# Optimization experiments

Measured on AMD Instinct MI355X. Metric: run time of the kernel, lower is better.

## Reference

```python
import jax, jax.numpy as jnp
import numpy as np

NUM_GRAPHS = 64

def setup_inputs() -> dict:
    key = jax.random.key(0)
    ks = jax.random.split(key, 10)
    N, E, D, V = 100000, 1600000, 64, 30
    node_types = jax.random.randint(ks[0], (N,), 0, V, dtype=jnp.int64 if jax.config.jax_enable_x64 else jnp.int32)
    edge_index = jax.random.randint(ks[1], (2, E), 0, N, dtype=jnp.int32)
    batch = jnp.sort(jax.random.randint(ks[2], (N,), 0, NUM_GRAPHS, dtype=jnp.int32))
    emb_table = jax.random.normal(ks[3], (V, D), dtype=jnp.float32)
    W1 = jax.random.normal(ks[4], (D, D), dtype=jnp.float32) / np.sqrt(D)
    W2 = jax.random.normal(ks[5], (D, D), dtype=jnp.float32) / np.sqrt(D)
    W3 = jax.random.normal(ks[6], (D, D), dtype=jnp.float32) / np.sqrt(D)
    b1 = jnp.zeros((D,), jnp.float32)
    b2 = jnp.zeros((D,), jnp.float32)
    b3 = jnp.zeros((D,), jnp.float32)
    return {"node_types": node_types, "edge_index": edge_index, "batch": batch,
            "emb_table": emb_table, "W1": W1, "b1": b1, "W2": W2, "b2": b2, "W3": W3, "b3": b3}

def _gcn_conv(x, W, b, row, col, norm, N):
    # x' = D^-1/2 (A+I) D^-1/2 (x @ W) + b   (PyG GCNConv semantics)
    h = x @ W
    msg = h[row] * norm[:, None]              # gather + edgewise scale
    out = jax.ops.segment_sum(msg, col, num_segments=N)  # scatter-add at targets
    return out + b

def reference(node_types, edge_index, batch, emb_table, W1, b1, W2, b2, W3, b3):
    N = node_types.shape[0]
    # add self-loops
    loops = jnp.arange(N, dtype=edge_index.dtype)
    row = jnp.concatenate([edge_index[0], loops])
    col = jnp.concatenate([edge_index[1], loops])
    # symmetric normalization on A + I
    deg = jax.ops.segment_sum(jnp.ones_like(col, dtype=jnp.float32), col, num_segments=N)
    dinv = jnp.where(deg > 0, jax.lax.rsqrt(deg), 0.0)
    norm = dinv[row] * dinv[col]
    x = emb_table[node_types]
    x = jax.nn.relu(_gcn_conv(x, W1, b1, row, col, norm, N))
    x = jax.nn.relu(_gcn_conv(x, W2, b2, row, col, norm, N))
    x = _gcn_conv(x, W3, b3, row, col, norm, N)
    # global mean pool over batch segments
    sums = jax.ops.segment_sum(x, batch, num_segments=NUM_GRAPHS)
    cnts = jax.ops.segment_sum(jnp.ones((N,), jnp.float32), batch, num_segments=NUM_GRAPHS)
    pooled = sums / jnp.maximum(cnts, 1.0)[:, None]
    # L2 normalize rows
    return pooled / jnp.linalg.norm(pooled, axis=1, keepdims=True)
```

## Files before the change

### kernel.cpp

```cpp
#include <hip/hip_runtime.h>
#include <hip/hip_fp16.h>

#define DD 64
#define NUM_GRAPHS 64
#define AGG_BLOCKS 2048
#define EB 512
#define BINW 256
#define MAXNB 512
#define EBIN_CAP 6144

typedef _Float16 h2_t __attribute__((ext_vector_type(2)));

__device__ __forceinline__ float fdot2u(unsigned a, unsigned b, float c) {
    return __builtin_amdgcn_fdot2(__builtin_bit_cast(h2_t, a),
                                  __builtin_bit_cast(h2_t, b), c, false);
}

#define MDLO(m) __half2float(__ushort_as_half((unsigned short)((m) & 0xFFFF)))

__global__ __launch_bounds__(256) void k_hist(const int* __restrict__ col,
                                              int* __restrict__ H, int E, int NB, int CE) {
    __shared__ int h[MAXNB];
    int eb = blockIdx.x, t = threadIdx.x;
    for (int i = t; i < NB; i += 256) h[i] = 0;
    __syncthreads();
    int e0 = eb * CE, e1 = min(E, e0 + CE);
    for (int e = e0 + t; e < e1; e += 256) atomicAdd(&h[col[e] >> 8], 1);
    __syncthreads();
    for (int i = t; i < NB; i += 256) H[eb * NB + i] = h[i];
}

__global__ __launch_bounds__(256) void k_scanA(int* __restrict__ H,
                                               int* __restrict__ bintot, int NB) {
    __shared__ int s[256];
    int b = blockIdx.x, t = threadIdx.x;
    int i0 = (2 * t) * NB + b, i1 = (2 * t + 1) * NB + b;
    int v0 = H[i0], v1 = H[i1];
    int tot = v0 + v1;
    s[t] = tot;
    __syncthreads();
    for (int off = 1; off < 256; off <<= 1) {
        int tv = (t >= off) ? s[t - off] : 0;
        __syncthreads();
        s[t] += tv;
        __syncthreads();
    }
    int excl = s[t] - tot;
    H[i0] = excl;
    H[i1] = excl + v0;
    if (t == 255) bintot[b] = s[255];
}

__global__ void k_scanB(const int* __restrict__ bintot, int* __restrict__ binstart, int NB) {
    __shared__ int s[512];
    int t = threadIdx.x;
    int v = (t < NB) ? bintot[t] : 0;
    s[t] = v;
    __syncthreads();
    for (int off = 1; off < 512; off <<= 1) {
        int tv = (t >= off) ? s[t - off] : 0;
        __syncthreads();
        s[t] += tv;
        __syncthreads();
    }
    if (t < NB) binstart[t] = s[t] - v;
    if (t == 511) binstart[NB] = s[511];
}

__global__ __launch_bounds__(256) void k_scatbin(const int* __restrict__ row,
                                                 const int* __restrict__ col,
                                                 const int* __restrict__ H,
                                                 const int* __restrict__ binstart,
                                                 unsigned* __restrict__ binned,
                                                 int E, int NB, int CE) {
    __shared__ int off[MAXNB];
    int eb = blockIdx.x, t = threadIdx.x;
    for (int i = t; i < NB; i += 256) off[i] = binstart[i] + H[eb * NB + i];
    __syncthreads();
    int e0 = eb * CE, e1 = min(E, e0 + CE);
    for (int e = e0 + t; e < e1; e += 256) {
        int c = col[e], r = row[e];
        int slot = atomicAdd(&off[c >> 8], 1);
        binned[slot] = ((unsigned)(c & 255) << 24) | (unsigned)r;
    }
}

__global__ __launch_bounds__(256) void k_bincsr(const unsigned* __restrict__ binned,
                                                const int* __restrict__ binstart,
                                                const int* __restrict__ nt,
                                                int* __restrict__ srcidx,
                                                int* __restrict__ rowptr,
                                                float* __restrict__ dinv,
                                                int2* __restrict__ pk, int N, int NB) {
    __shared__ unsigned arr[EBIN_CAP];
    __shared__ int sorted_[EBIN_CAP];
    __shared__ int cnt[BINW];
    __shared__ int base[BINW];
    __shared__ int cursor[BINW];
    int b = blockIdx.x, t = threadIdx.x;
    int s0 = binstart[b], s1 = binstart[b + 1];
    int binsz = s1 - s0;
    if (binsz > EBIN_CAP) binsz = EBIN_CAP;
    cnt[t] = 0;
    for (int i = t; i < binsz; i += 256) arr[i] = binned[s0 + i];
    __syncthreads();
    for (int i = t; i < binsz; i += 256) atomicAdd(&cnt[arr[i] >> 24], 1);
    __syncthreads();
    int v = cnt[t];
    base[t] = v;
    __syncthreads();
    for (int off = 1; off < 256; off <<= 1) {
        int tv = (t >= off) ? base[t - off] : 0;
        __syncthreads();
        base[t] += tv;
        __syncthreads();
    }
    int excl = base[t] - v;
    __syncthreads();
    base[t] = excl;
    cursor[t] = excl;
    __syncthreads();
    for (int i = t; i < binsz; i += 256) {
        unsigned val = arr[i];
        int pos = atomicAdd(&cursor[val >> 24], 1);
        sorted_[pos] = (int)(val & 0xFFFFFF);
    }
    __syncthreads();
    for (int i = t; i < binsz; i += 256) srcidx[s0 + i] = sorted_[i];
    int node = b * BINW + t;
    if (node < N) {
        rowptr[node] = s0 + base[t];
        float di = rsqrtf((float)cnt[t] + 1.0f);
        dinv[node] = di;
        pk[node] = make_int2(nt[node], __float_as_int(di));
    }
    if (b == NB - 1 && t == 0) rowptr[N] = s1;
}

__global__ void k_buildepk(const int* __restrict__ srcidx, const int2* __restrict__ pk,
                           unsigned* __restrict__ epku, int E) {
    int i = blockIdx.x * blockDim.x + threadIdx.x;
    if (i >= E) return;
    int2 p = pk[srcidx[i]];
    epku[i] = ((unsigned)p.x << 16) |
              (unsigned)__half_as_ushort(__float2half(__int_as_float(p.y)));
}

__global__ void k_embW1(const float* __restrict__ emb, const float* __restrict__ W1,
                        float* __restrict__ embW1, int V) {
    __shared__ float er[DD];
    int v = blockIdx.x, j = threadIdx.x;
    er[j] = emb[v * DD + j];
    __syncthreads();
    float acc = 0.0f;
    #pragma unroll
    for (int d = 0; d < DD; ++d) acc += er[d] * W1[d * DD + j];
    embW1[v * DD + j] = acc;
}

__global__ void k_packW(const float* __restrict__ W, unsigned* __restrict__ Wpk) {
    int t = blockIdx.x * blockDim.x + threadIdx.x;
    if (t >= 32 * DD) return;
    int p = t >> 6, j = t & 63;
    __half2 h = __floats2half2_rn(W[(2 * p) * DD + j], W[(2 * p + 1) * DD + j]);
    Wpk[t] = __builtin_bit_cast(unsigned, h);
}

__device__ __forceinline__ void acc_h4(float4& a, uint2 r) {
    float2 f0 = __half22float2(*(const __half2*)&r.x);
    float2 f1 = __half22float2(*(const __half2*)&r.y);
    a.x += f0.x; a.y += f0.y; a.z += f1.x; a.w += f1.y;
}

__device__ __forceinline__ float4 gather_partial_q(const int* __restrict__ srcidx,
                                                   const __half* __restrict__ Hs,
                                                   int s, int e, int g, int l) {
    float4 A = {0,0,0,0}, B = {0,0,0,0}, C = {0,0,0,0}, D = {0,0,0,0};
    int k = s;
    int kend = s + ((e - s) & ~15);
    if (k < kend) {
        uint2 r0 = *(const uint2*)(Hs + (long)srcidx[k + g] * DD + 4 * l);
        uint2 r1 = *(const uint2*)(Hs + (long)srcidx[k + 4 + g] * DD + 4 * l);
        uint2 r2 = *(const uint2*)(Hs + (long)srcidx[k + 8 + g] * DD + 4 * l);
        uint2 r3 = *(const uint2*)(Hs + (long)srcidx[k + 12 + g] * DD + 4 * l);
        k += 16;
        for (; k < kend; k += 16) {
            uint2 n0 = *(const uint2*)(Hs + (long)srcidx[k + g] * DD + 4 * l);
            uint2 n1 = *(const uint2*)(Hs + (long)srcidx[k + 4 + g] * DD + 4 * l);
            uint2 n2 = *(const uint2*)(Hs + (long)srcidx[k + 8 + g] * DD + 4 * l);
            uint2 n3 = *(const uint2*)(Hs + (long)srcidx[k + 12 + g] * DD + 4 * l);
            acc_h4(A, r0); acc_h4(B, r1); acc_h4(C, r2); acc_h4(D, r3);
            r0 = n0; r1 = n1; r2 = n2; r3 = n3;
        }
        acc_h4(A, r0); acc_h4(B, r1); acc_h4(C, r2); acc_h4(D, r3);
    }
    for (; k < e; k += 4) {
        if (k + g < e) {
            uint2 rr = *(const uint2*)(Hs + (long)srcidx[k + g] * DD + 4 * l);
            acc_h4(A, rr);
        }
    }
    A.x += B.x + C.x + D.x; A.y += B.y + C.y + D.y;
    A.z += B.z + C.z + D.z; A.w += B.w + C.w + D.w;
    return A;
}

__device__ __forceinline__ void acc_h8(float4& A, float4& B, uint4 r) {
    float2 f0 = __half22float2(*(const __half2*)&r.x);
    float2 f1 = __half22float2(*(const __half2*)&r.y);
    float2 f2 = __half22float2(*(const __half2*)&r.z);
    float2 f3 = __half22float2(*(const __half2*)&r.w);
    A.x += f0.x; A.y += f0.y; A.z += f1.x; A.w += f1.y;
    B.x += f2.x; B.y += f2.y; B.z += f3.x; B.w += f3.y;
}

__device__ __forceinline__ void gather_sum_8p(const int* __restrict__ srcidx,
                                              const __half* __restrict__ Hs,
                                              int s, int e, int g, int l,
                                              float4& A, float4& B, int pi0, int pi1) {
    float4 A1 = {0.f, 0.f, 0.f, 0.f}, B1 = {0.f, 0.f, 0.f, 0.f};
    int k = s;
    int kend = s + ((e - s) & ~15);
    if (k < kend) {
        uint4 r0 = *(const uint4*)(Hs + (long)pi0 * DD + 8 * l);
        uint4 r1 = *(const uint4*)(Hs + (long)pi1 * DD + 8 * l);
        k += 16;
        for (; k < kend; k += 16) {
            uint4 n0 = *(const uint4*)(Hs + (long)srcidx[k + g] * DD + 8 * l);
            uint4 n1 = *(const uint4*)(Hs + (long)srcidx[k + 8 + g] * DD + 8 * l);
            acc_h8(A, B, r0);
            acc_h8(A1, B1, r1);
            r0 = n0; r1 = n1;
        }
        acc_h8(A, B, r0);
        acc_h8(A1, B1, r1);
    }
    if (k + 8 <= e) {
        uint4 r = *(const uint4*)(Hs + (long)srcidx[k + g] * DD + 8 * l);
        acc_h8(A, B, r);
        k += 8;
    }
    if (k + g < e) {
        uint4 r = *(const uint4*)(Hs + (long)srcidx[k + g] * DD + 8 * l);
        acc_h8(A1, B1, r);
    }
    A.x += A1.x; A.y += A1.y; A.z += A1.z; A.w += A1.w;
    B.x += B1.x; B.y += B1.y; B.z += B1.z; B.w += B1.w;
}

__global__ __launch_bounds__(256, 4) void k_agg1_fused(const int* __restrict__ rowptr,
                                                    const unsigned* __restrict__ epku,
                                                    const int2* __restrict__ pk,
                                                    const float* __restrict__ embW1,
                                                    const float* __restrict__ b1,
                                                    __half* __restrict__ OUT, int N, int V) {
    __shared__ float ew[30 * DD];
    int tid = threadIdx.x;
    for (int k = tid; k < V * DD; k += 256) ew[k] = embW1[k];
    __syncthreads();
    int lane = tid & 63;
    int g = lane >> 4, l = lane & 15;
    float4 bq = *(const float4*)(b1 + 4 * l);
    int wstride = gridDim.x * 4;
    int node = __builtin_amdgcn_readfirstlane(blockIdx.x * 4 + (tid >> 6));
    int s = 0, e = 0;
    unsigned pu0 = 0, pu1 = 0;
    if (node < N) {
        s = rowptr[node]; e = rowptr[node + 1];
        if (e - s >= 8) { pu0 = epku[s + g]; pu1 = epku[s + 4 + g]; }
    }
#define P8(U0, U1) { \
        unsigned _u0 = (U0), _u1 = (U1); \
        int _t0 = _u0 >> 16, _t1 = _u1 >> 16; \
        float _d0 = MDLO(_u0), _d1 = MDLO(_u1); \
        float4 _w0 = *(const float4*)(ew + _t0 * DD + 4 * l); \
        float4 _w1 = *(const float4*)(ew + _t1 * DD + 4 * l); \
        acc.x += _w0.x * _d0 + _w1.x * _d1; \
        acc.y += _w0.y * _d0 + _w1.y * _d1; \
        acc.z += _w0.z * _d0 + _w1.z * _d1; \
        acc.w += _w0.w * _d0 + _w1.w * _d1; }
#define P4(U0) { \
        unsigned _u0 = (U0); \
        int _t0 = _u0 >> 16; \
        float _d0 = MDLO(_u0); \
        float4 _w0 = *(const float4*)(ew + _t0 * DD + 4 * l); \
        acc.x += _w0.x * _d0; acc.y += _w0.y * _d0; \
        acc.z += _w0.z * _d0; acc.w += _w0.w * _d0; }
    while (node < N) {
        int nn = node + wstride;
        int ns = 0, ne = 0;
        if (nn < N) { ns = rowptr[nn]; ne = rowptr[nn + 1]; }
        int2 pc = pk[node];
        float4 acc = {0.f, 0.f, 0.f, 0.f};
        int k = s;
        if (k + 8 <= e) {
            P8(pu0, pu1);
            k += 8;
            for (; k + 8 <= e; k += 8) P8(epku[k + g], epku[k + 4 + g]);
        }
        if (k + 4 <= e) { P4(epku[k + g]); k += 4; }
        if (k + g < e)  { P4(epku[k + g]); }
        unsigned npu0 = 0, npu1 = 0;
        if (nn < N && ne - ns >= 8) { npu0 = epku[ns + g]; npu1 = epku[ns + 4 + g]; }
        acc.x += __shfl_xor(acc.x, 16, 64); acc.x += __shfl_xor(acc.x, 32, 64);
        acc.y += __shfl_xor(acc.y, 16, 64); acc.y += __shfl_xor(acc.y, 32, 64);
        acc.z += __shfl_xor(acc.z, 16, 64); acc.z += __shfl_xor(acc.z, 32, 64);
        acc.w += __shfl_xor(acc.w, 16, 64); acc.w += __shfl_xor(acc.w, 32, 64);
        float dc = __int_as_float(pc.y);
        float4 wc = *(const float4*)(ew + pc.x * DD + 4 * l);
        float4 v;
        v.x = fmaxf((acc.x + wc.x * dc) * dc + bq.x, 0.f) * dc;
        v.y = fmaxf((acc.y + wc.y * dc) * dc + bq.y, 0.f) * dc;
        v.z = fmaxf((acc.z + wc.z * dc) * dc + bq.z, 0.f) * dc;
        v.w = fmaxf((acc.w + wc.w * dc) * dc + bq.w, 0.f) * dc;
        if (g == 0) {
            __half2 h0 = __floats2half2_rn(v.x, v.y);
            __half2 h1 = __floats2half2_rn(v.z, v.w);
            uint2 st;
            st.x = __builtin_bit_cast(unsigned, h0);
            st.y = __builtin_bit_cast(unsigned, h1);
            *(uint2*)(OUT + (long)node * DD + 4 * l) = st;
        }
        node = nn; s = ns; e = ne; pu0 = npu0; pu1 = npu1;
    }
#undef P8
#undef P4
}

__global__ __launch_bounds__(256, 4) void k_agg2_fused(const int* __restrict__ rowptr,
                                                    const int* __restrict__ srcidx,
                                                    const float* __restrict__ dinv,
                                                    const __half* __restrict__ Hs,
                                                    const float* __restrict__ b2,
                                                    const unsigned* __restrict__ W2pk,
                                                    __half* __restrict__ OUT, int N) {
    int tid = threadIdx.x;
    int lane = tid & 63;
    int g = lane >> 3, l = lane & 7;
    unsigned Wc[32];
    #pragma unroll
    for (int p = 0; p < 32; ++p) Wc[p] = W2pk[p * DD + lane];
    float bl = b2[lane];
    int wstride = gridDim.x * 4;
    int node = __builtin_amdgcn_readfirstlane(blockIdx.x * 4 + (tid >> 6));
    int s = 0, e = 0;
    int pi0 = 0, pi1 = 0;
    if (node < N) {
        s = rowptr[node]; e = rowptr[node + 1];
        if (e - s >= 16) { pi0 = srcidx[s + g]; pi1 = srcidx[s + 8 + g]; }
    }
    while (node < N) {
        int nn = node + wstride;
        int ns = 0, ne = 0;
        if (nn < N) { ns = rowptr[nn]; ne = rowptr[nn + 1]; }
        float dc = dinv[node];
        uint4 sr = *(const uint4*)(Hs + (long)node * DD + 8 * l);
        float4 A = {0.f, 0.f, 0.f, 0.f}, B = {0.f, 0.f, 0.f, 0.f};
        gather_sum_8p(srcidx, Hs, s, e, g, l, A, B, pi0, pi1);
        int npi0 = 0, npi1 = 0;
        if (nn < N && ne - ns >= 16) { npi0 = srcidx[ns + g]; npi1 = srcidx[ns + 8 + g]; }
        #pragma unroll
        for (int m = 8; m <= 32; m <<= 1) {
            A.x += __shfl_xor(A.x, m, 64); A.y += __shfl_xor(A.y, m, 64);
            A.z += __shfl_xor(A.z, m, 64); A.w += __shfl_xor(A.w, m, 64);
            B.x += __shfl_xor(B.x, m, 64); B.y += __shfl_xor(B.y, m, 64);
            B.z += __shfl_xor(B.z, m, 64); B.w += __shfl_xor(B.w, m, 64);
        }
        float2 s0 = __half22float2(*(const __half2*)&sr.x);
        float2 s1 = __half22float2(*(const __half2*)&sr.y);
        float2 s2 = __half22float2(*(const __half2*)&sr.z);
        float2 s3 = __half22float2(*(const __half2*)&sr.w);
        float t0 = (A.x + s0.x) * dc, t1 = (A.y + s0.y) * dc;
        float t2 = (A.z + s1.x) * dc, t3 = (A.w + s1.y) * dc;
        float t4 = (B.x + s2.x) * dc, t5 = (B.y + s2.y) * dc;
        float t6 = (B.z + s3.x) * dc, t7 = (B.w + s3.y) * dc;
        int vp0 = __builtin_bit_cast(int, __floats2half2_rn(t0, t1));
        int vp1 = __builtin_bit_cast(int, __floats2half2_rn(t2, t3));
        int vp2 = __builtin_bit_cast(int, __floats2half2_rn(t4, t5));
        int vp3 = __builtin_bit_cast(int, __floats2half2_rn(t6, t7));
        float o0 = 0.f, o1 = 0.f, o2 = 0.f, o3 = 0.f;
        #pragma unroll
        for (int p = 0; p < 32; p += 4) {
            o0 = fdot2u((unsigned)__builtin_amdgcn_readlane(vp0, p >> 2), Wc[p + 0], o0);
            o1 = fdot2u((unsigned)__builtin_amdgcn_readlane(vp1, p >> 2), Wc[p + 1], o1);
            o2 = fdot2u((unsigned)__builtin_amdgcn_readlane(vp2, p >> 2), Wc[p + 2], o2);
            o3 = fdot2u((unsigned)__builtin_amdgcn_readlane(vp3, p >> 2), Wc[p + 3], o3);
        }
        float u = (o0 + o1) + (o2 + o3);
        float v2 = fmaxf(u + bl, 0.f);
        OUT[(long)node * DD + lane] = __float2half(v2 * dc);
        node = nn; s = ns; e = ne; pi0 = npi0; pi1 = npi1;
    }
}

__device__ __forceinline__ void flush_pool_q(float4& PA, float* __restrict__ pool,
                                             int gcur, int g, int l) {
    gcur &= (NUM_GRAPHS - 1);
    PA.x += __shfl_xor(PA.x, 16, 64); PA.x += __shfl_xor(PA.x, 32, 64);
    PA.y += __shfl_xor(PA.y, 16, 64); PA.y += __shfl_xor(PA.y, 32, 64);
    PA.z += __shfl_xor(PA.z, 16, 64); PA.z += __shfl_xor(PA.z, 32, 64);
    PA.w += __shfl_xor(PA.w, 16, 64); PA.w += __shfl_xor(PA.w, 32, 64);
    if (g == 0) {
        atomicAdd(&pool[gcur * DD + 4 * l + 0], PA.x);
        atomicAdd(&pool[gcur * DD + 4 * l + 1], PA.y);
        atomicAdd(&pool[gcur * DD + 4 * l + 2], PA.z);
        atomicAdd(&pool[gcur * DD + 4 * l + 3], PA.w);
    }
}

__global__ __launch_bounds__(256, 4) void k_agg3_pool(const int* __restrict__ rowptr,
                                                   const int* __restrict__ srcidx,
                                                   const float* __restrict__ dinv,
                                                   const __half* __restrict__ Hs,
                                                   const int* __restrict__ batch,
                                                   float* __restrict__ pool,
                                                   int N, int chunk) {
    int tid = threadIdx.x;
    int lane = tid & 63;
    int g = lane >> 4, l = lane & 15;
    int w = __builtin_amdgcn_readfirstlane(blockIdx.x * 4 + (tid >> 6));
    int start = w * chunk;
    if (start >= N) return;
    int endn = min(N, start + chunk);
    int gcur = batch[start];
    float4 PA = {0.f, 0.f, 0.f, 0.f};
    int s = rowptr[start];
    for (int node = start; node < endn; ++node) {
        int e = rowptr[node + 1];
        float dc = dinv[node];
        int gb = batch[node];
        uint2 sr = *(const uint2*)(Hs + (long)node * DD + 4 * l);
        float4 A = gather_partial_q(srcidx, Hs, s, e, g, l);
        if (g == 0) {
            float2 s0 = __half22float2(*(const __half2*)&sr.x);
            float2 s1 = __half22float2(*(const __half2*)&sr.y);
            A.x += s0.x; A.y += s0.y; A.z += s1.x; A.w += s1.y;
        }
        if (gb != gcur) {
            flush_pool_q(PA, pool, gcur, g, l);
            gcur = gb;
            PA.x = dc * A.x; PA.y = dc * A.y; PA.z = dc * A.z; PA.w = dc * A.w;
        } else {
            PA.x += dc * A.x; PA.y += dc * A.y; PA.z += dc * A.z; PA.w += dc * A.w;
        }
        s = e;
    }
    flush_pool_q(PA, pool, gcur, g, l);
}

__global__ void k_final(const float* __restrict__ pool, const int* __restrict__ batch,
                        const float* __restrict__ W3, const float* __restrict__ b3,
                        float* __restrict__ out, int N) {
    __shared__ float pr[DD];
    int g = blockIdx.x, j = threadIdx.x;
    pr[j] = pool[g * DD + j];
    __syncthreads();
    int lo = 0, hi = N;
    while (lo < hi) { int m = (lo + hi) >> 1; if (batch[m] < g) lo = m + 1; else hi = m; }
    int lo2 = lo; hi = N;
    while (lo2 < hi) { int m = (lo2 + hi) >> 1; if (batch[m] < g + 1) lo2 = m + 1; else hi = m; }
    float cnt = fmaxf((float)(lo2 - lo), 1.0f);
    float acc = 0.0f;
    #pragma unroll
    for (int d = 0; d < DD; ++d) acc += pr[d] * W3[d * DD + j];
    float v = acc / cnt + b3[j];
    float sq = v * v;
    #pragma unroll
    for (int off = 32; off > 0; off >>= 1) sq += __shfl_down(sq, off, 64);
    float nrm = __shfl(sq, 0, 64);
    out[g * DD + j] = v / sqrtf(nrm);
}

extern "C" void kernel_launch(void* const* d_in, const int* in_sizes, int n_in,
                              void* d_out, int out_size, void* d_ws, size_t ws_size,
                              hipStream_t stream) {
    const int*   node_types = (const int*)d_in[0];
    const int*   edge_index = (const int*)d_in[1];
    const int*   batch      = (const int*)d_in[2];
    const float* emb        = (const float*)d_in[3];
    const float* W1 = (const float*)d_in[4];
    const float* b1 = (const float*)d_in[5];
    const float* W2 = (const float*)d_in[6];
    const float* b2 = (const float*)d_in[7];
    const float* W3 = (const float*)d_in[8];
    const float* b3 = (const float*)d_in[9];
    const int N = in_sizes[0];
    const int E = in_sizes[1] / 2;
    const int V = in_sizes[3] / DD;
    const int* row = edge_index;
    const int* col = edge_index + E;
    const long ND = (long)N * DD;
    const int NB = (N + BINW - 1) / BINW;
    const int CE = (E + EB - 1) / EB;

    char* p = (char*)d_ws;
    __half*   hsA     = (__half*)p;       p += ND * sizeof(__half);
    __half*   hsB     = (__half*)p;       p += ND * sizeof(__half);
    int*      srcidx  = (int*)p;          p += (size_t)E * sizeof(int);
    unsigned* epku    = (unsigned*)p;     p += (size_t)E * sizeof(unsigned);
    unsigned* binned  = (unsigned*)p;     p += (size_t)E * sizeof(unsigned);
    int*      H       = (int*)p;          p += (size_t)EB * NB * sizeof(int);
    int*      bintot  = (int*)p;          p += (size_t)(NB + 4) * sizeof(int);
    int*      binstart= (int*)p;          p += (size_t)(NB + 4) * sizeof(int);
    float*    dinv    = (float*)p;        p += (size_t)N * sizeof(float);
    int2*     pk      = (int2*)p;         p += (size_t)N * sizeof(int2);
    int*      rowptr  = (int*)p;          p += (size_t)(N + 4) * sizeof(int);
    float*    pool    = (float*)p;        p += (size_t)NUM_GRAPHS * DD * sizeof(float);
    float*    embW1   = (float*)p;        p += (size_t)V * DD * sizeof(float);
    unsigned* W2pk    = (unsigned*)p;     p += 32 * DD * sizeof(unsigned);

    k_hist<<<EB, 256, 0, stream>>>(col, H, E, NB, CE);
    k_scanA<<<NB, 256, 0, stream>>>(H, bintot, NB);
    k_scanB<<<1, 512, 0, stream>>>(bintot, binstart, NB);
    k_scatbin<<<EB, 256, 0, stream>>>(row, col, H, binstart, binned, E, NB, CE);
    k_bincsr<<<NB, 256, 0, stream>>>(binned, binstart, node_types, srcidx, rowptr,
                                     dinv, pk, N, NB);
    k_buildepk<<<(E + 255) / 256, 256, 0, stream>>>(srcidx, pk, epku, E);

    k_embW1<<<V, DD, 0, stream>>>(emb, W1, embW1, V);
    k_packW<<<8, 256, 0, stream>>>(W2, W2pk);

    k_agg1_fused<<<AGG_BLOCKS, 256, 0, stream>>>(rowptr, epku, pk, embW1, b1,
                                                 hsA, N, V);
    k_agg2_fused<<<AGG_BLOCKS, 256, 0, stream>>>(rowptr, srcidx, dinv, hsA, b2, W2pk,
                                                 hsB, N);
    hipMemsetAsync(pool, 0, (size_t)(NUM_GRAPHS * DD) * sizeof(float), stream);
    const int totalWaves = AGG_BLOCKS * 4;
    const int chunk = (N + totalWaves - 1) / totalWaves;
    k_agg3_pool<<<AGG_BLOCKS, 256, 0, stream>>>(rowptr, srcidx, dinv, hsB, batch,
                                                pool, N, chunk);
    k_final<<<NUM_GRAPHS, DD, 0, stream>>>(pool, batch, W3, b3, (float*)d_out, N);
}
```

Before: 276.2 us.

## Predicate gathers with zero sentinel row and prefetch next node's neighbors

Replaces the tail-handling branches in the three aggregation kernels with predicated loads. Out-of-range edges read a zeroed sentinel row at index N (or a zero packed word in layer 1). The layer-2 and layer-3 kernels also software-pipeline across nodes: the first 16 neighbor rows of the next node are loaded while the current node is reduced. This is meant to hide gather latency and remove divergent remainder loops, at the cost of wasted loads for low-degree nodes, extra registers, and two extra memsets with padded buffers.

```diff
diff --git a/kernel.cpp b/kernel.cpp
--- a/kernel.cpp
+++ b/kernel.cpp
@@ -171,40 +171,6 @@
     float2 f1 = __half22float2(*(const __half2*)&r.y);
     a.x += f0.x; a.y += f0.y; a.z += f1.x; a.w += f1.y;
 }
-
-__device__ __forceinline__ float4 gather_partial_q(const int* __restrict__ srcidx,
-                                                   const __half* __restrict__ Hs,
-                                                   int s, int e, int g, int l) {
-    float4 A = {0,0,0,0}, B = {0,0,0,0}, C = {0,0,0,0}, D = {0,0,0,0};
-    int k = s;
-    int kend = s + ((e - s) & ~15);
-    if (k < kend) {
-        uint2 r0 = *(const uint2*)(Hs + (long)srcidx[k + g] * DD + 4 * l);
-        uint2 r1 = *(const uint2*)(Hs + (long)srcidx[k + 4 + g] * DD + 4 * l);
-        uint2 r2 = *(const uint2*)(Hs + (long)srcidx[k + 8 + g] * DD + 4 * l);
-        uint2 r3 = *(const uint2*)(Hs + (long)srcidx[k + 12 + g] * DD + 4 * l);
-        k += 16;
-        for (; k < kend; k += 16) {
-            uint2 n0 = *(const uint2*)(Hs + (long)srcidx[k + g] * DD + 4 * l);
-            uint2 n1 = *(const uint2*)(Hs + (long)srcidx[k + 4 + g] * DD + 4 * l);
-            uint2 n2 = *(const uint2*)(Hs + (long)srcidx[k + 8 + g] * DD + 4 * l);
-            uint2 n3 = *(const uint2*)(Hs + (long)srcidx[k + 12 + g] * DD + 4 * l);
-            acc_h4(A, r0); acc_h4(B, r1); acc_h4(C, r2); acc_h4(D, r3);
-            r0 = n0; r1 = n1; r2 = n2; r3 = n3;
-        }
-        acc_h4(A, r0); acc_h4(B, r1); acc_h4(C, r2); acc_h4(D, r3);
-    }
-    for (; k < e; k += 4) {
-        if (k + g < e) {
-            uint2 rr = *(const uint2*)(Hs + (long)srcidx[k + g] * DD + 4 * l);
-            acc_h4(A, rr);
-        }
-    }
-    A.x += B.x + C.x + D.x; A.y += B.y + C.y + D.y;
-    A.z += B.z + C.z + D.z; A.w += B.w + C.w + D.w;
-    return A;
-}
-
 __device__ __forceinline__ void acc_h8(float4& A, float4& B, uint4 r) {
     float2 f0 = __half22float2(*(const __half2*)&r.x);
     float2 f1 = __half22float2(*(const __half2*)&r.y);
@@ -212,40 +178,6 @@
     float2 f3 = __half22float2(*(const __half2*)&r.w);
     A.x += f0.x; A.y += f0.y; A.z += f1.x; A.w += f1.y;
     B.x += f2.x; B.y += f2.y; B.z += f3.x; B.w += f3.y;
-}
-
-__device__ __forceinline__ void gather_sum_8p(const int* __restrict__ srcidx,
-                                              const __half* __restrict__ Hs,
-                                              int s, int e, int g, int l,
-                                              float4& A, float4& B, int pi0, int pi1) {
-    float4 A1 = {0.f, 0.f, 0.f, 0.f}, B1 = {0.f, 0.f, 0.f, 0.f};
-    int k = s;
-    int kend = s + ((e - s) & ~15);
-    if (k < kend) {
-        uint4 r0 = *(const uint4*)(Hs + (long)pi0 * DD + 8 * l);
-        uint4 r1 = *(const uint4*)(Hs + (long)pi1 * DD + 8 * l);
-        k += 16;
-        for (; k < kend; k += 16) {
-            uint4 n0 = *(const uint4*)(Hs + (long)srcidx[k + g] * DD + 8 * l);
-            uint4 n1 = *(const uint4*)(Hs + (long)srcidx[k + 8 + g] * DD + 8 * l);
-            acc_h8(A, B, r0);
-            acc_h8(A1, B1, r1);
-            r0 = n0; r1 = n1;
-        }
-        acc_h8(A, B, r0);
-        acc_h8(A1, B1, r1);
-    }
-    if (k + 8 <= e) {
-        uint4 r = *(const uint4*)(Hs + (long)srcidx[k + g] * DD + 8 * l);
-        acc_h8(A, B, r);
-        k += 8;
-    }
-    if (k + g < e) {
-        uint4 r = *(const uint4*)(Hs + (long)srcidx[k + g] * DD + 8 * l);
-        acc_h8(A1, B1, r);
-    }
-    A.x += A1.x; A.y += A1.y; A.z += A1.z; A.w += A1.w;
-    B.x += B1.x; B.y += B1.y; B.z += B1.z; B.w += B1.w;
 }
 
 __global__ __launch_bounds__(256, 4) void k_agg1_fused(const int* __restrict__ rowptr,
@@ -267,7 +199,9 @@
     unsigned pu0 = 0, pu1 = 0;
     if (node < N) {
         s = rowptr[node]; e = rowptr[node + 1];
-        if (e - s >= 8) { pu0 = epku[s + g]; pu1 = epku[s + 4 + g]; }
+        unsigned a0 = epku[s + g], a1 = epku[s + 4 + g];
+        pu0 = (s + g < e) ? a0 : 0u;
+        pu1 = (s + 4 + g < e) ? a1 : 0u;
     }
 #define P8(U0, U1) { \
         unsigned _u0 = (U0), _u1 = (U1); \
@@ -279,29 +213,26 @@
         acc.y += _w0.y * _d0 + _w1.y * _d1; \
         acc.z += _w0.z * _d0 + _w1.z * _d1; \
         acc.w += _w0.w * _d0 + _w1.w * _d1; }
-#define P4(U0) { \
-        unsigned _u0 = (U0); \
-        int _t0 = _u0 >> 16; \
-        float _d0 = MDLO(_u0); \
-        float4 _w0 = *(const float4*)(ew + _t0 * DD + 4 * l); \
-        acc.x += _w0.x * _d0; acc.y += _w0.y * _d0; \
-        acc.z += _w0.z * _d0; acc.w += _w0.w * _d0; }
     while (node < N) {
         int nn = node + wstride;
         int ns = 0, ne = 0;
         if (nn < N) { ns = rowptr[nn]; ne = rowptr[nn + 1]; }
         int2 pc = pk[node];
         float4 acc = {0.f, 0.f, 0.f, 0.f};
-        int k = s;
-        if (k + 8 <= e) {
-            P8(pu0, pu1);
-            k += 8;
-            for (; k + 8 <= e; k += 8) P8(epku[k + g], epku[k + 4 + g]);
-        }
-        if (k + 4 <= e) { P4(epku[k + g]); k += 4; }
-        if (k + g < e)  { P4(epku[k + g]); }
+        P8(pu0, pu1);
+        int eR = s + ((e - s + 7) & ~7);
+        for (int k = s + 8; k < eR; k += 8) {
+            unsigned a0 = epku[k + g], a1 = epku[k + 4 + g];
+            unsigned u0 = (k + g < e) ? a0 : 0u;
+            unsigned u1 = (k + 4 + g < e) ? a1 : 0u;
+            P8(u0, u1);
+        }
         unsigned npu0 = 0, npu1 = 0;
-        if (nn < N && ne - ns >= 8) { npu0 = epku[ns + g]; npu1 = epku[ns + 4 + g]; }
+        if (nn < N) {
+            unsigned a0 = epku[ns + g], a1 = epku[ns + 4 + g];
+            npu0 = (ns + g < ne) ? a0 : 0u;
+            npu1 = (ns + 4 + g < ne) ? a1 : 0u;
+        }
         acc.x += __shfl_xor(acc.x, 16, 64); acc.x += __shfl_xor(acc.x, 32, 64);
         acc.y += __shfl_xor(acc.y, 16, 64); acc.y += __shfl_xor(acc.y, 32, 64);
         acc.z += __shfl_xor(acc.z, 16, 64); acc.z += __shfl_xor(acc.z, 32, 64);
@@ -324,7 +255,6 @@
         node = nn; s = ns; e = ne; pu0 = npu0; pu1 = npu1;
     }
 #undef P8
-#undef P4
 }
 
 __global__ __launch_bounds__(256, 4) void k_agg2_fused(const int* __restrict__ rowptr,
@@ -343,22 +273,47 @@
     float bl = b2[lane];
     int wstride = gridDim.x * 4;
     int node = __builtin_amdgcn_readfirstlane(blockIdx.x * 4 + (tid >> 6));
-    int s = 0, e = 0;
-    int pi0 = 0, pi1 = 0;
+    int nn = node + wstride;
+    int s = 0, e = 0, ns = 0, ne = 0;
+    uint4 cr0 = {0, 0, 0, 0}, cr1 = {0, 0, 0, 0};
     if (node < N) {
         s = rowptr[node]; e = rowptr[node + 1];
-        if (e - s >= 16) { pi0 = srcidx[s + g]; pi1 = srcidx[s + 8 + g]; }
-    }
+        int i0 = (s + g < e) ? srcidx[s + g] : N;
+        int i1 = (s + 8 + g < e) ? srcidx[s + 8 + g] : N;
+        cr0 = *(const uint4*)(Hs + (long)i0 * DD + 8 * l);
+        cr1 = *(const uint4*)(Hs + (long)i1 * DD + 8 * l);
+    }
+    if (nn < N) { ns = rowptr[nn]; ne = rowptr[nn + 1]; }
     while (node < N) {
-        int nn = node + wstride;
-        int ns = 0, ne = 0;
-        if (nn < N) { ns = rowptr[nn]; ne = rowptr[nn + 1]; }
+        int n2 = nn + wstride;
+        int s2 = 0, e2 = 0;
+        if (n2 < N) { s2 = rowptr[n2]; e2 = rowptr[n2 + 1]; }
+        uint4 nr0 = {0, 0, 0, 0}, nr1 = {0, 0, 0, 0};
+        if (nn < N) {
+            int i0 = (ns + g < ne) ? srcidx[ns + g] : N;
+            int i1 = (ns + 8 + g < ne) ? srcidx[ns + 8 + g] : N;
+            nr0 = *(const uint4*)(Hs + (long)i0 * DD + 8 * l);
+            nr1 = *(const uint4*)(Hs + (long)i1 * DD + 8 * l);
+        }
         float dc = dinv[node];
         uint4 sr = *(const uint4*)(Hs + (long)node * DD + 8 * l);
         float4 A = {0.f, 0.f, 0.f, 0.f}, B = {0.f, 0.f, 0.f, 0.f};
-        gather_sum_8p(srcidx, Hs, s, e, g, l, A, B, pi0, pi1);
-        int npi0 = 0, npi1 = 0;
-        if (nn < N && ne - ns >= 16) { npi0 = srcidx[ns + g]; npi1 = srcidx[ns + 8 + g]; }
+        float4 A1 = {0.f, 0.f, 0.f, 0.f}, B1 = {0.f, 0.f, 0.f, 0.f};
+        uint4 r0 = cr0, r1 = cr1;
+        int eR = s + ((e - s + 15) & ~15);
+        for (int k = s + 16; k < eR; k += 16) {
+            int i0 = (k + g < e) ? srcidx[k + g] : N;
+            int i1 = (k + 8 + g < e) ? srcidx[k + 8 + g] : N;
+            uint4 n0 = *(const uint4*)(Hs + (long)i0 * DD + 8 * l);
+            uint4 n1 = *(const uint4*)(Hs + (long)i1 * DD + 8 * l);
+            acc_h8(A, B, r0);
+            acc_h8(A1, B1, r1);
+            r0 = n0; r1 = n1;
+        }
+        acc_h8(A, B, r0);
+        acc_h8(A1, B1, r1);
+        A.x += A1.x; A.y += A1.y; A.z += A1.z; A.w += A1.w;
+        B.x += B1.x; B.y += B1.y; B.z += B1.z; B.w += B1.w;
         #pragma unroll
         for (int m = 8; m <= 32; m <<= 1) {
             A.x += __shfl_xor(A.x, m, 64); A.y += __shfl_xor(A.y, m, 64);
@@ -368,11 +323,11 @@
         }
         float2 s0 = __half22float2(*(const __half2*)&sr.x);
         float2 s1 = __half22float2(*(const __half2*)&sr.y);
-        float2 s2 = __half22float2(*(const __half2*)&sr.z);
+        float2 s2f = __half22float2(*(const __half2*)&sr.z);
         float2 s3 = __half22float2(*(const __half2*)&sr.w);
         float t0 = (A.x + s0.x) * dc, t1 = (A.y + s0.y) * dc;
         float t2 = (A.z + s1.x) * dc, t3 = (A.w + s1.y) * dc;
-        float t4 = (B.x + s2.x) * dc, t5 = (B.y + s2.y) * dc;
+        float t4 = (B.x + s2f.x) * dc, t5 = (B.y + s2f.y) * dc;
         float t6 = (B.z + s3.x) * dc, t7 = (B.w + s3.y) * dc;
         int vp0 = __builtin_bit_cast(int, __floats2half2_rn(t0, t1));
         int vp1 = __builtin_bit_cast(int, __floats2half2_rn(t2, t3));
@@ -389,7 +344,9 @@
         float u = (o0 + o1) + (o2 + o3);
         float v2 = fmaxf(u + bl, 0.f);
         OUT[(long)node * DD + lane] = __float2half(v2 * dc);
-        node = nn; s = ns; e = ne; pi0 = npi0; pi1 = npi1;
+        node = nn; s = ns; e = ne;
+        nn = n2; ns = s2; ne = e2;
+        cr0 = nr0; cr1 = nr1;
     }
 }
 
@@ -425,12 +382,51 @@
     int gcur = batch[start];
     float4 PA = {0.f, 0.f, 0.f, 0.f};
     int s = rowptr[start];
+    int e = rowptr[start + 1];
+    uint2 cr0, cr1, cr2, cr3;
+    {
+        int i0 = (s + g < e) ? srcidx[s + g] : N;
+        int i1 = (s + 4 + g < e) ? srcidx[s + 4 + g] : N;
+        int i2 = (s + 8 + g < e) ? srcidx[s + 8 + g] : N;
+        int i3 = (s + 12 + g < e) ? srcidx[s + 12 + g] : N;
+        cr0 = *(const uint2*)(Hs + (long)i0 * DD + 4 * l);
+        cr1 = *(const uint2*)(Hs + (long)i1 * DD + 4 * l);
+        cr2 = *(const uint2*)(Hs + (long)i2 * DD + 4 * l);
+        cr3 = *(const uint2*)(Hs + (long)i3 * DD + 4 * l);
+    }
     for (int node = start; node < endn; ++node) {
-        int e = rowptr[node + 1];
+        int ns = e;
+        int nep = rowptr[min(node + 2, N)];
+        int ne = (node + 1 < endn) ? nep : ns;
+        int j0 = (ns + g < ne) ? srcidx[ns + g] : N;
+        int j1 = (ns + 4 + g < ne) ? srcidx[ns + 4 + g] : N;
+        int j2 = (ns + 8 + g < ne) ? srcidx[ns + 8 + g] : N;
+        int j3 = (ns + 12 + g < ne) ? srcidx[ns + 12 + g] : N;
+        uint2 nr0 = *(const uint2*)(Hs + (long)j0 * DD + 4 * l);
+        uint2 nr1 = *(const uint2*)(Hs + (long)j1 * DD + 4 * l);
+        uint2 nr2 = *(const uint2*)(Hs + (long)j2 * DD + 4 * l);
+        uint2 nr3 = *(const uint2*)(Hs + (long)j3 * DD + 4 * l);
         float dc = dinv[node];
         int gb = batch[node];
         uint2 sr = *(const uint2*)(Hs + (long)node * DD + 4 * l);
-        float4 A = gather_partial_q(srcidx, Hs, s, e, g, l);
+        float4 A = {0,0,0,0}, B = {0,0,0,0}, C = {0,0,0,0}, D = {0,0,0,0};
+        uint2 r0 = cr0, r1 = cr1, r2 = cr2, r3 = cr3;
+        int eR = s + ((e - s + 15) & ~15);
+        for (int k = s + 16; k < eR; k += 16) {
+            int i0 = (k + g < e) ? srcidx[k + g] : N;
+            int i1 = (k + 4 + g < e) ? srcidx[k + 4 + g] : N;
+            int i2 = (k + 8 + g < e) ? srcidx[k + 8 + g] : N;
+            int i3 = (k + 12 + g < e) ? srcidx[k + 12 + g] : N;
+            uint2 n0 = *(const uint2*)(Hs + (long)i0 * DD + 4 * l);
+            uint2 n1 = *(const uint2*)(Hs + (long)i1 * DD + 4 * l);
+            uint2 n2 = *(const uint2*)(Hs + (long)i2 * DD + 4 * l);
+            uint2 n3 = *(const uint2*)(Hs + (long)i3 * DD + 4 * l);
+            acc_h4(A, r0); acc_h4(B, r1); acc_h4(C, r2); acc_h4(D, r3);
+            r0 = n0; r1 = n1; r2 = n2; r3 = n3;
+        }
+        acc_h4(A, r0); acc_h4(B, r1); acc_h4(C, r2); acc_h4(D, r3);
+        A.x += B.x + C.x + D.x; A.y += B.y + C.y + D.y;
+        A.z += B.z + C.z + D.z; A.w += B.w + C.w + D.w;
         if (g == 0) {
             float2 s0 = __half22float2(*(const __half2*)&sr.x);
             float2 s1 = __half22float2(*(const __half2*)&sr.y);
@@ -443,7 +439,8 @@
         } else {
             PA.x += dc * A.x; PA.y += dc * A.y; PA.z += dc * A.z; PA.w += dc * A.w;
         }
-        s = e;
+        s = ns; e = ne;
+        cr0 = nr0; cr1 = nr1; cr2 = nr2; cr3 = nr3;
     }
     flush_pool_q(PA, pool, gcur, g, l);
 }
@@ -494,10 +491,10 @@
     const int CE = (E + EB - 1) / EB;
 
     char* p = (char*)d_ws;
-    __half*   hsA     = (__half*)p;       p += ND * sizeof(__half);
-    __half*   hsB     = (__half*)p;       p += ND * sizeof(__half);
-    int*      srcidx  = (int*)p;          p += (size_t)E * sizeof(int);
-    unsigned* epku    = (unsigned*)p;     p += (size_t)E * sizeof(unsigned);
+    __half*   hsA     = (__half*)p;       p += (ND + DD) * sizeof(__half);
+    __half*   hsB     = (__half*)p;       p += (ND + DD) * sizeof(__half);
+    int*      srcidx  = (int*)p;          p += (size_t)(E + 64) * sizeof(int);
+    unsigned* epku    = (unsigned*)p;     p += (size_t)(E + 64) * sizeof(unsigned);
     unsigned* binned  = (unsigned*)p;     p += (size_t)E * sizeof(unsigned);
     int*      H       = (int*)p;          p += (size_t)EB * NB * sizeof(int);
     int*      bintot  = (int*)p;          p += (size_t)(NB + 4) * sizeof(int);
@@ -509,6 +506,9 @@
     float*    embW1   = (float*)p;        p += (size_t)V * DD * sizeof(float);
     unsigned* W2pk    = (unsigned*)p;     p += 32 * DD * sizeof(unsigned);
 
+    hipMemsetAsync(hsA + ND, 0, DD * sizeof(__half), stream);
+    hipMemsetAsync(hsB + ND, 0, DD * sizeof(__half), stream);
+
     k_hist<<<EB, 256, 0, stream>>>(col, H, E, NB, CE);
     k_scanA<<<NB, 256, 0, stream>>>(H, bintot, NB);
     k_scanB<<<1, 512, 0, stream>>>(bintot, binstart, NB);
```

Result: slower. 292.5 us (+5.9%).
